# Kernel optimization log

Measured on AMD Instinct MI355X. Metric: run time of the kernel, lower is better.

Reference implementation:

```python
import jax, jax.numpy as jnp
import numpy as np

N_NODES = 100000
N_EDGES = 640000
D_IN = 128
D_HID = 128
D_OUT = 64


def gcn_conv(x, src, dst, ew, W, b, num_nodes):
    """GCNConv with add_self_loops=False: h = D^{-1/2} A D^{-1/2} (x W) + b.

    PyG gcn_norm: row, col = edge_index; deg = scatter_add(edge_weight, col);
    norm = deg^{-1/2}[row] * ew * deg^{-1/2}[col]; aggregate messages into col.
    """
    h = x @ W  # [N, d_out]
    deg = jax.ops.segment_sum(ew, dst, num_segments=num_nodes)  # [N]
    dinv = jnp.where(deg > 0, jax.lax.rsqrt(deg), 0.0)
    norm = dinv[src] * ew * dinv[dst]  # [E]
    out = jax.ops.segment_sum(norm[:, None] * h[src], dst, num_segments=num_nodes)
    return out + b


def setup_inputs() -> dict:
    key = jax.random.key(0)
    ks = jax.random.split(key, 9)
    x = jax.random.normal(ks[0], (N_NODES, D_IN), dtype=jnp.float32)
    edge_index = jax.random.randint(ks[1], (2, N_EDGES), 0, N_NODES, dtype=jnp.int64)
    edge_weight = jax.random.uniform(ks[2], (N_EDGES,), dtype=jnp.float32)
    def glorot(k, fan_in, fan_out):
        s = jnp.sqrt(6.0 / (fan_in + fan_out))
        return jax.random.uniform(k, (fan_in, fan_out), minval=-s, maxval=s, dtype=jnp.float32)
    W1 = glorot(ks[3], D_IN, D_HID); b1 = jnp.zeros((D_HID,), jnp.float32)
    W2 = glorot(ks[4], D_HID, D_HID); b2 = jnp.zeros((D_HID,), jnp.float32)
    W3 = glorot(ks[5], D_HID, D_OUT); b3 = jnp.zeros((D_OUT,), jnp.float32)
    return {"x": x, "edge_index": edge_index, "edge_weight": edge_weight,
            "W1": W1, "b1": b1, "W2": W2, "b2": b2, "W3": W3, "b3": b3}


def reference(x, edge_index, edge_weight, W1, b1, W2, b2, W3, b3):
    src, dst = edge_index[0], edge_index[1]
    n = x.shape[0]
    embeddings = []
    h = gcn_conv(x, src, dst, edge_weight, W1, b1, n)
    h = jax.nn.relu(h)
    embeddings.append(h)
    h = gcn_conv(h, src, dst, edge_weight, W2, b2, n)
    h = jax.nn.relu(h)
    embeddings.append(h)
    h = gcn_conv(h, src, dst, edge_weight, W3, b3, n)
    embeddings.append(h)
    return tuple(embeddings)
```

## Files before the change

kernel.cpp:

```cpp
#include <hip/hip_runtime.h>

#define NN 100000
#define NE 640000

typedef unsigned int uint32;
typedef __attribute__((ext_vector_type(8))) short short8;
typedef __attribute__((ext_vector_type(4))) float f32x4;

static __device__ __forceinline__ ushort f2bf(float f) {
    uint32 u = __float_as_uint(f);
    u = (u + 0x7fffu + ((u >> 16) & 1u)) >> 16;
    return (ushort)u;
}
static __device__ __forceinline__ float bf2f(uint32 bits16) {
    return __uint_as_float(bits16 << 16);
}
static __device__ __forceinline__ uint32 pack2(float a, float b) {
    return (uint32)f2bf(a) | ((uint32)f2bf(b) << 16);
}


__global__ void k_deg_hist(const int* __restrict__ dst, const float* __restrict__ ew,
                           float* __restrict__ deg, int* __restrict__ cnt, int E) {
    int e = blockIdx.x * blockDim.x + threadIdx.x;
    if (e < E) {
        int d = dst[e];
        atomicAdd(&deg[d], ew[e]);
        atomicAdd(&cnt[d], 1);
    }
}


__global__ void k_scan1(const int* __restrict__ cnt, int* __restrict__ rp,
                        int* __restrict__ bsum, int n) {
    __shared__ int tsum[256];
    const int base = blockIdx.x * 1024;
    const int t = threadIdx.x;
    int v[4], s = 0;
#pragma unroll
    for (int j = 0; j < 4; ++j) {
        int idx = base + t * 4 + j;
        v[j] = (idx < n) ? cnt[idx] : 0;
        s += v[j];
    }
    tsum[t] = s;
    __syncthreads();
    for (int off = 1; off < 256; off <<= 1) {
        int x = (t >= off) ? tsum[t - off] : 0;
        __syncthreads();
        tsum[t] += x;
        __syncthreads();
    }
    int excl = (t > 0) ? tsum[t - 1] : 0;
#pragma unroll
    for (int j = 0; j < 4; ++j) {
        int idx = base + t * 4 + j;
        if (idx < n) rp[idx] = excl;
        excl += v[j];
    }
    if (t == 255) bsum[blockIdx.x] = tsum[255];
}

__global__ void k_scan2(int* __restrict__ bsum, int nb) {
    __shared__ int sh[256];
    int t = threadIdx.x;
    sh[t] = (t < nb) ? bsum[t] : 0;
    __syncthreads();
    for (int off = 1; off < 256; off <<= 1) {
        int x = (t >= off) ? sh[t - off] : 0;
        __syncthreads();
        sh[t] += x;
        __syncthreads();
    }
    if (t < nb) bsum[t] = (t > 0) ? sh[t - 1] : 0;
}

__global__ void k_scan3(int* __restrict__ rp, const int* __restrict__ bsum,
                        int* __restrict__ cursor, float* __restrict__ deg, int n) {
    int i = blockIdx.x * blockDim.x + threadIdx.x;
    if (i < n) {
        int v = rp[i] + bsum[i >> 10];
        rp[i] = v;
        cursor[i] = v;
        float d = deg[i];
        deg[i] = (d > 0.f) ? rsqrtf(d) : 0.f;
    }
    if (i == 0) rp[n] = NE;
}

__global__ void k_fill(const int* __restrict__ src, const int* __restrict__ dst,
                       const float* __restrict__ ew, const float* __restrict__ dinv,
                       int* __restrict__ cursor, uint2* __restrict__ ep, int E) {
    int e = blockIdx.x * blockDim.x + threadIdx.x;
    if (e < E) {
        int s = src[e], d = dst[e];
        int pos = atomicAdd(&cursor[d], 1);
        float nv = dinv[s] * ew[e] * dinv[d];
        ep[pos] = make_uint2((uint32)s, __float_as_uint(nv));
    }
}

__global__ void k_prepW_all(const float* __restrict__ W1, const float* __restrict__ W2,
                            const float* __restrict__ W3, ushort* __restrict__ wt1,
                            ushort* __restrict__ wt2, ushort* __restrict__ wt3) {
    int o = blockIdx.x * blockDim.x + threadIdx.x;
    if (o < 16384) {
        int col = o >> 7, k = o & 127;
        wt1[o] = f2bf(W1[k * 128 + col]);
    } else if (o < 32768) {
        int oo = o - 16384;
        int col = oo >> 7, k = oo & 127;
        wt2[oo] = f2bf(W2[k * 128 + col]);
    } else if (o < 40960) {
        int oo = o - 32768;
        int col = oo >> 7, k = oo & 127;
        wt3[oo] = f2bf(W3[k * 64 + col]);
    }
}

template <int NOUT>
__global__ __launch_bounds__(256) void k_gemm_mfma(const float* __restrict__ X,
                                                   const ushort* __restrict__ Wt,
                                                   ushort* __restrict__ H, int N) {
    __shared__ char smem[64 * 256 + NOUT * 256];
    char* xs = smem;
    char* wt = smem + 64 * 256;
    const int tid = threadIdx.x;
    const int row0 = blockIdx.x * 64;

    const uint4* Wt4 = reinterpret_cast<const uint4*>(Wt);
#pragma unroll
    for (int i = 0; i < NOUT / 16; ++i) {
        int id = tid + 256 * i;
        int col = id >> 4, c4 = id & 15;
        uint4 v = Wt4[id];
        *reinterpret_cast<uint4*>(wt + col * 256 + ((c4 * 16) ^ ((col & 7) << 4))) = v;
    }
#pragma unroll
    for (int i = 0; i < 8; ++i) {
        int id = tid + 256 * i;
        int r = id >> 5, c4 = id & 31;
        int gr = row0 + r;
        float4 v = make_float4(0.f, 0.f, 0.f, 0.f);
        if (gr < N) v = *reinterpret_cast<const float4*>(&X[(size_t)gr * 128 + c4 * 4]);
        uint2 pk;
        pk.x = pack2(v.x, v.y);
        pk.y = pack2(v.z, v.w);
        *reinterpret_cast<uint2*>(xs + r * 256 + ((c4 * 8) ^ ((r & 7) << 4))) = pk;
    }
    __syncthreads();

    const int w = tid >> 6, lane = tid & 63;
    const int rl = w * 16 + (lane & 15);
    const int kg = lane >> 4;
    f32x4 acc[NOUT / 16];
#pragma unroll
    for (int ct = 0; ct < NOUT / 16; ++ct) acc[ct] = (f32x4){0.f, 0.f, 0.f, 0.f};

#pragma unroll
    for (int ks = 0; ks < 4; ++ks) {
        const int kb = ks * 64 + kg * 16;
        short8 a = *reinterpret_cast<const short8*>(xs + rl * 256 + (kb ^ ((rl & 7) << 4)));
#pragma unroll
        for (int ct = 0; ct < NOUT / 16; ++ct) {
            int col = ct * 16 + (lane & 15);
            short8 bfr = *reinterpret_cast<const short8*>(wt + col * 256 + (kb ^ ((col & 7) << 4)));
            acc[ct] = __builtin_amdgcn_mfma_f32_16x16x32_bf16(a, bfr, acc[ct], 0, 0, 0);
        }
    }
#pragma unroll
    for (int ct = 0; ct < NOUT / 16; ++ct) {
        int col = ct * 16 + (lane & 15);
#pragma unroll
        for (int r = 0; r < 4; ++r) {
            int gr = row0 + w * 16 + (lane >> 4) * 4 + r;
            if (gr < N) H[(size_t)gr * NOUT + col] = f2bf(acc[ct][r]);
        }
    }
}

template <int WAVES, int RELU>
__global__ void k_agg128(const int* __restrict__ rp, const uint2* __restrict__ ep,
                         const ushort* __restrict__ H, const float* __restrict__ b,
                         float* __restrict__ out, int N) {
    const int wave = threadIdx.x >> 6;
    const int lane = threadIdx.x & 63;
    const int n = blockIdx.x * WAVES + wave;
    if (n >= N) return;
    const int e0 = rp[n], e1 = rp[n + 1];
    const int slot = lane >> 4;
    const int l16 = lane & 15;

    const float4 b0 = *reinterpret_cast<const float4*>(&b[l16 * 8]);
    const float4 b1 = *reinterpret_cast<const float4*>(&b[l16 * 8 + 4]);

    float a[8] = {};
    int e = e0 + slot;
    if (e < e1) {
        uint2 p = ep[e];
        for (;;) {
            const int en = e + 4;
            uint2 pn = ep[en];
            float w = __uint_as_float(p.y);
            uint4 hv = *reinterpret_cast<const uint4*>(&H[(size_t)p.x * 128 + l16 * 8]);
            a[0] = fmaf(w, bf2f(hv.x & 0xffffu), a[0]);
            a[1] = fmaf(w, bf2f(hv.x >> 16), a[1]);
            a[2] = fmaf(w, bf2f(hv.y & 0xffffu), a[2]);
            a[3] = fmaf(w, bf2f(hv.y >> 16), a[3]);
            a[4] = fmaf(w, bf2f(hv.z & 0xffffu), a[4]);
            a[5] = fmaf(w, bf2f(hv.z >> 16), a[5]);
            a[6] = fmaf(w, bf2f(hv.w & 0xffffu), a[6]);
            a[7] = fmaf(w, bf2f(hv.w >> 16), a[7]);
            e = en;
            if (e >= e1) break;
            p = pn;
        }
    }
#pragma unroll
    for (int j = 0; j < 8; ++j) {
        a[j] += __shfl_xor(a[j], 32);
        a[j] += __shfl_xor(a[j], 16);
    }
    if (lane < 16) {
        float4 o0 = make_float4(a[0] + b0.x, a[1] + b0.y, a[2] + b0.z, a[3] + b0.w);
        float4 o1 = make_float4(a[4] + b1.x, a[5] + b1.y, a[6] + b1.z, a[7] + b1.w);
        if (RELU) {
            o0.x = fmaxf(o0.x, 0.f); o0.y = fmaxf(o0.y, 0.f);
            o0.z = fmaxf(o0.z, 0.f); o0.w = fmaxf(o0.w, 0.f);
            o1.x = fmaxf(o1.x, 0.f); o1.y = fmaxf(o1.y, 0.f);
            o1.z = fmaxf(o1.z, 0.f); o1.w = fmaxf(o1.w, 0.f);
        }
        float* op = &out[(size_t)n * 128 + l16 * 8];
        *reinterpret_cast<float4*>(op) = o0;
        *reinterpret_cast<float4*>(op + 4) = o1;
    }
}

template <int WAVES, int RELU>
__global__ void k_agg64(const int* __restrict__ rp, const uint2* __restrict__ ep,
                        const ushort* __restrict__ H, const float* __restrict__ b,
                        float* __restrict__ out, int N) {
    const int wave = threadIdx.x >> 6;
    const int lane = threadIdx.x & 63;
    const int n = blockIdx.x * WAVES + wave;
    if (n >= N) return;
    const int e0 = rp[n], e1 = rp[n + 1];
    const int slot = lane >> 3;
    const int l8 = lane & 7;

    const float4 b0 = *reinterpret_cast<const float4*>(&b[l8 * 8]);
    const float4 b1 = *reinterpret_cast<const float4*>(&b[l8 * 8 + 4]);

    float a[8] = {};
    int e = e0 + slot;
    if (e < e1) {
        uint2 p = ep[e];
        for (;;) {
            const int en = e + 8;
            uint2 pn = ep[en];
            float w = __uint_as_float(p.y);
            uint4 hv = *reinterpret_cast<const uint4*>(&H[(size_t)p.x * 64 + l8 * 8]);
            a[0] = fmaf(w, bf2f(hv.x & 0xffffu), a[0]);
            a[1] = fmaf(w, bf2f(hv.x >> 16), a[1]);
            a[2] = fmaf(w, bf2f(hv.y & 0xffffu), a[2]);
            a[3] = fmaf(w, bf2f(hv.y >> 16), a[3]);
            a[4] = fmaf(w, bf2f(hv.z & 0xffffu), a[4]);
            a[5] = fmaf(w, bf2f(hv.z >> 16), a[5]);
            a[6] = fmaf(w, bf2f(hv.w & 0xffffu), a[6]);
            a[7] = fmaf(w, bf2f(hv.w >> 16), a[7]);
            e = en;
            if (e >= e1) break;
            p = pn;
        }
    }
#pragma unroll
    for (int j = 0; j < 8; ++j) {
        a[j] += __shfl_xor(a[j], 8);
        a[j] += __shfl_xor(a[j], 16);
        a[j] += __shfl_xor(a[j], 32);
    }
    if (lane < 8) {
        float4 o0 = make_float4(a[0] + b0.x, a[1] + b0.y, a[2] + b0.z, a[3] + b0.w);
        float4 o1 = make_float4(a[4] + b1.x, a[5] + b1.y, a[6] + b1.z, a[7] + b1.w);
        if (RELU) {
            o0.x = fmaxf(o0.x, 0.f); o0.y = fmaxf(o0.y, 0.f);
            o0.z = fmaxf(o0.z, 0.f); o0.w = fmaxf(o0.w, 0.f);
            o1.x = fmaxf(o1.x, 0.f); o1.y = fmaxf(o1.y, 0.f);
            o1.z = fmaxf(o1.z, 0.f); o1.w = fmaxf(o1.w, 0.f);
        }
        float* op = &out[(size_t)n * 64 + l8 * 8];
        *reinterpret_cast<float4*>(op) = o0;
        *reinterpret_cast<float4*>(op + 4) = o1;
    }
}


extern "C" void kernel_launch(void* const* d_in, const int* in_sizes, int n_in,
                              void* d_out, int out_size, void* d_ws, size_t ws_size,
                              hipStream_t stream) {
    const float* x  = (const float*)d_in[0];
    const int*   ei = (const int*)d_in[1];
    const float* ew = (const float*)d_in[2];
    const float* W1 = (const float*)d_in[3];
    const float* b1 = (const float*)d_in[4];
    const float* W2 = (const float*)d_in[5];
    const float* b2 = (const float*)d_in[6];
    const float* W3 = (const float*)d_in[7];
    const float* b3 = (const float*)d_in[8];

    const int* src = ei;
    const int* dst = ei + NE;

    float*  ws    = (float*)d_ws;
    float*  deg   = ws;
    int*    cnt   = (int*)(ws + NN);
    int*    rp    = (int*)(ws + 2 * NN);
    int*    bsum  = (int*)(ws + 3 * NN + 64);
    uint2*  ep    = (uint2*)(ws + 3 * NN + 256);
    ushort* h1    = (ushort*)(ws + 3 * NN + 256 + 2 * NE);
    ushort* h2    = h1 + (size_t)NN * 128;
    ushort* h3    = h1;
    ushort* wt1   = h2 + (size_t)NN * 128;
    ushort* wt2   = wt1 + 128 * 128;
    ushort* wt3   = wt2 + 128 * 128;

    float* out0 = (float*)d_out;
    float* out1 = out0 + NN * 128;
    float* out2 = out1 + NN * 128;

    const int B = 256;
    const int NB_SCAN = (NN + 1023) / 1024;

    k_prepW_all<<<(40960 + B - 1) / B, B, 0, stream>>>(W1, W2, W3, wt1, wt2, wt3);

    hipMemsetAsync(deg, 0, 2 * NN * sizeof(float), stream);
    k_deg_hist<<<(NE + B - 1) / B, B, 0, stream>>>(dst, ew, deg, cnt, NE);
    k_scan1<<<NB_SCAN, 256, 0, stream>>>(cnt, rp, bsum, NN);
    k_scan2<<<1, 256, 0, stream>>>(bsum, NB_SCAN);
    k_scan3<<<(NN + B - 1) / B, B, 0, stream>>>(rp, bsum, cnt, deg, NN);
    k_fill<<<(NE + B - 1) / B, B, 0, stream>>>(src, dst, ew, deg, cnt, ep, NE);

    const int GB = (NN + 63) / 64;

    k_gemm_mfma<128><<<GB, 256, 0, stream>>>(x, wt1, h1, NN);
    k_agg128<4, 1><<<(NN + 3) / 4, 256, 0, stream>>>(rp, ep, h1, b1, out0, NN);

    k_gemm_mfma<128><<<GB, 256, 0, stream>>>(out0, wt2, h2, NN);
    k_agg128<4, 1><<<(NN + 3) / 4, 256, 0, stream>>>(rp, ep, h2, b2, out1, NN);

    k_gemm_mfma<64><<<GB, 256, 0, stream>>>(out1, wt3, h3, NN);
    k_agg64<4, 0><<<(NN + 3) / 4, 256, 0, stream>>>(rp, ep, h3, b3, out2, NN);
}
```

Before: 278.6 us.

## Fuse weight prep with zeroing and co-launch degree histogram with first GEMM

Folds the degree/count memset into the weight-conversion kernel, and merges the degree histogram into the first GEMM launch as extra blocks, so the independent histogram atomics overlap with the layer-1 GEMM. The histogram now processes four edges per thread with vector loads. This cuts two launches and the serial dependency of histogram then GEMM. The catch is larger shared memory for the histogram blocks, which may lower occupancy, and contention between atomics and GEMM traffic.

```diff
diff --git a/kernel.cpp b/kernel.cpp
--- a/kernel.cpp
+++ b/kernel.cpp
@@ -2,6 +2,10 @@
 
 #define NN 100000
 #define NE 640000
+#define GB1 ((NN + 63) / 64)
+#define HB1 (NE / 4 / 256)
+#define PWB 160
+#define ZB  ((2 * NN + 255) / 256)
 
 typedef unsigned int uint32;
 typedef __attribute__((ext_vector_type(8))) short short8;
@@ -19,15 +23,120 @@
     return (uint32)f2bf(a) | ((uint32)f2bf(b) << 16);
 }
 
-
-__global__ void k_deg_hist(const int* __restrict__ dst, const float* __restrict__ ew,
-                           float* __restrict__ deg, int* __restrict__ cnt, int E) {
-    int e = blockIdx.x * blockDim.x + threadIdx.x;
-    if (e < E) {
-        int d = dst[e];
-        atomicAdd(&deg[d], ew[e]);
-        atomicAdd(&cnt[d], 1);
-    }
+__global__ void k_prep_zero(const float* __restrict__ W1, const float* __restrict__ W2,
+                            const float* __restrict__ W3, ushort* __restrict__ wt1,
+                            ushort* __restrict__ wt2, ushort* __restrict__ wt3,
+                            int* __restrict__ degcnt) {
+    const int b = blockIdx.x;
+    if (b < PWB) {
+        int o = b * 256 + threadIdx.x;
+        if (o < 16384) {
+            int col = o >> 7, k = o & 127;
+            wt1[o] = f2bf(W1[k * 128 + col]);
+        } else if (o < 32768) {
+            int oo = o - 16384;
+            int col = oo >> 7, k = oo & 127;
+            wt2[oo] = f2bf(W2[k * 128 + col]);
+        } else if (o < 40960) {
+            int oo = o - 32768;
+            int col = oo >> 7, k = oo & 127;
+            wt3[oo] = f2bf(W3[k * 64 + col]);
+        }
+    } else {
+        int i = (b - PWB) * 256 + threadIdx.x;
+        if (i < 2 * NN) degcnt[i] = 0;
+    }
+}
+
+template <int NOUT>
+static __device__ __forceinline__ void gemm_body(const float* __restrict__ X,
+                                                 const ushort* __restrict__ Wt,
+                                                 ushort* __restrict__ H, int N,
+                                                 int bid, int tid, char* smem) {
+    char* xs = smem;
+    char* wt = smem + 64 * 256;
+    const int row0 = bid * 64;
+
+    const uint4* Wt4 = reinterpret_cast<const uint4*>(Wt);
+#pragma unroll
+    for (int i = 0; i < NOUT / 16; ++i) {
+        int id = tid + 256 * i;
+        int col = id >> 4, c4 = id & 15;
+        uint4 v = Wt4[id];
+        *reinterpret_cast<uint4*>(wt + col * 256 + ((c4 * 16) ^ ((col & 7) << 4))) = v;
+    }
+#pragma unroll
+    for (int i = 0; i < 8; ++i) {
+        int id = tid + 256 * i;
+        int r = id >> 5, c4 = id & 31;
+        int gr = row0 + r;
+        float4 v = make_float4(0.f, 0.f, 0.f, 0.f);
+        if (gr < N) v = *reinterpret_cast<const float4*>(&X[(size_t)gr * 128 + c4 * 4]);
+        uint2 pk;
+        pk.x = pack2(v.x, v.y);
+        pk.y = pack2(v.z, v.w);
+        *reinterpret_cast<uint2*>(xs + r * 256 + ((c4 * 8) ^ ((r & 7) << 4))) = pk;
+    }
+    __syncthreads();
+
+    const int w = tid >> 6, lane = tid & 63;
+    const int rl = w * 16 + (lane & 15);
+    const int kg = lane >> 4;
+    f32x4 acc[NOUT / 16];
+#pragma unroll
+    for (int ct = 0; ct < NOUT / 16; ++ct) acc[ct] = (f32x4){0.f, 0.f, 0.f, 0.f};
+
+#pragma unroll
+    for (int ks = 0; ks < 4; ++ks) {
+        const int kb = ks * 64 + kg * 16;
+        short8 a = *reinterpret_cast<const short8*>(xs + rl * 256 + (kb ^ ((rl & 7) << 4)));
+#pragma unroll
+        for (int ct = 0; ct < NOUT / 16; ++ct) {
+            int col = ct * 16 + (lane & 15);
+            short8 bfr = *reinterpret_cast<const short8*>(wt + col * 256 + (kb ^ ((col & 7) << 4)));
+            acc[ct] = __builtin_amdgcn_mfma_f32_16x16x32_bf16(a, bfr, acc[ct], 0, 0, 0);
+        }
+    }
+#pragma unroll
+    for (int ct = 0; ct < NOUT / 16; ++ct) {
+        int col = ct * 16 + (lane & 15);
+#pragma unroll
+        for (int r = 0; r < 4; ++r) {
+            int gr = row0 + w * 16 + (lane >> 4) * 4 + r;
+            if (gr < N) H[(size_t)gr * NOUT + col] = f2bf(acc[ct][r]);
+        }
+    }
+}
+
+__global__ __launch_bounds__(256) void k_gemm1_hist(const float* __restrict__ X,
+                                                    const ushort* __restrict__ Wt1,
+                                                    ushort* __restrict__ H, int N,
+                                                    const int* __restrict__ dst,
+                                                    const float* __restrict__ ew,
+                                                    float* __restrict__ deg,
+                                                    int* __restrict__ cnt) {
+    __shared__ char smem[64 * 256 + 128 * 256];
+    if (blockIdx.x < GB1) {
+        gemm_body<128>(X, Wt1, H, N, blockIdx.x, threadIdx.x, smem);
+    } else {
+        int e0 = ((blockIdx.x - GB1) * 256 + threadIdx.x) * 4;
+        if (e0 < NE) {
+            int4 d4 = *reinterpret_cast<const int4*>(&dst[e0]);
+            float4 w4 = *reinterpret_cast<const float4*>(&ew[e0]);
+            atomicAdd(&deg[d4.x], w4.x); atomicAdd(&cnt[d4.x], 1);
+            atomicAdd(&deg[d4.y], w4.y); atomicAdd(&cnt[d4.y], 1);
+            atomicAdd(&deg[d4.z], w4.z); atomicAdd(&cnt[d4.z], 1);
+            atomicAdd(&deg[d4.w], w4.w); atomicAdd(&cnt[d4.w], 1);
+        }
+    }
+}
+
+template <int NOUT>
+__global__ __launch_bounds__(256) void k_gemm_mfma(const float* __restrict__ X,
+                                                   const ushort* __restrict__ Wt,
+                                                   ushort* __restrict__ H, int N) {
+    __shared__ char smem[64 * 256 + NOUT * 256];
+    gemm_body<NOUT>(X, Wt, H, N, blockIdx.x, threadIdx.x, smem);
 }
 
 
@@ -97,85 +206,6 @@
         int pos = atomicAdd(&cursor[d], 1);
         float nv = dinv[s] * ew[e] * dinv[d];
         ep[pos] = make_uint2((uint32)s, __float_as_uint(nv));
-    }
-}
-
-__global__ void k_prepW_all(const float* __restrict__ W1, const float* __restrict__ W2,
-                            const float* __restrict__ W3, ushort* __restrict__ wt1,
-                            ushort* __restrict__ wt2, ushort* __restrict__ wt3) {
-    int o = blockIdx.x * blockDim.x + threadIdx.x;
-    if (o < 16384) {
-        int col = o >> 7, k = o & 127;
-        wt1[o] = f2bf(W1[k * 128 + col]);
-    } else if (o < 32768) {
-        int oo = o - 16384;
-        int col = oo >> 7, k = oo & 127;
-        wt2[oo] = f2bf(W2[k * 128 + col]);
-    } else if (o < 40960) {
-        int oo = o - 32768;
-        int col = oo >> 7, k = oo & 127;
-        wt3[oo] = f2bf(W3[k * 64 + col]);
-    }
-}
-
-template <int NOUT>
-__global__ __launch_bounds__(256) void k_gemm_mfma(const float* __restrict__ X,
-                                                   const ushort* __restrict__ Wt,
-                                                   ushort* __restrict__ H, int N) {
-    __shared__ char smem[64 * 256 + NOUT * 256];
-    char* xs = smem;
-    char* wt = smem + 64 * 256;
-    const int tid = threadIdx.x;
-    const int row0 = blockIdx.x * 64;
-
-    const uint4* Wt4 = reinterpret_cast<const uint4*>(Wt);
-#pragma unroll
-    for (int i = 0; i < NOUT / 16; ++i) {
-        int id = tid + 256 * i;
-        int col = id >> 4, c4 = id & 15;
-        uint4 v = Wt4[id];
-        *reinterpret_cast<uint4*>(wt + col * 256 + ((c4 * 16) ^ ((col & 7) << 4))) = v;
-    }
-#pragma unroll
-    for (int i = 0; i < 8; ++i) {
-        int id = tid + 256 * i;
-        int r = id >> 5, c4 = id & 31;
-        int gr = row0 + r;
-        float4 v = make_float4(0.f, 0.f, 0.f, 0.f);
-        if (gr < N) v = *reinterpret_cast<const float4*>(&X[(size_t)gr * 128 + c4 * 4]);
-        uint2 pk;
-        pk.x = pack2(v.x, v.y);
-        pk.y = pack2(v.z, v.w);
-        *reinterpret_cast<uint2*>(xs + r * 256 + ((c4 * 8) ^ ((r & 7) << 4))) = pk;
-    }
-    __syncthreads();
-
-    const int w = tid >> 6, lane = tid & 63;
-    const int rl = w * 16 + (lane & 15);
-    const int kg = lane >> 4;
-    f32x4 acc[NOUT / 16];
-#pragma unroll
-    for (int ct = 0; ct < NOUT / 16; ++ct) acc[ct] = (f32x4){0.f, 0.f, 0.f, 0.f};
-
-#pragma unroll
-    for (int ks = 0; ks < 4; ++ks) {
-        const int kb = ks * 64 + kg * 16;
-        short8 a = *reinterpret_cast<const short8*>(xs + rl * 256 + (kb ^ ((rl & 7) << 4)));
-#pragma unroll
-        for (int ct = 0; ct < NOUT / 16; ++ct) {
-            int col = ct * 16 + (lane & 15);
-            short8 bfr = *reinterpret_cast<const short8*>(wt + col * 256 + (kb ^ ((col & 7) << 4)));
-            acc[ct] = __builtin_amdgcn_mfma_f32_16x16x32_bf16(a, bfr, acc[ct], 0, 0, 0);
-        }
-    }
-#pragma unroll
-    for (int ct = 0; ct < NOUT / 16; ++ct) {
-        int col = ct * 16 + (lane & 15);
-#pragma unroll
-        for (int r = 0; r < 4; ++r) {
-            int gr = row0 + w * 16 + (lane >> 4) * 4 + r;
-            if (gr < N) H[(size_t)gr * NOUT + col] = f2bf(acc[ct][r]);
-        }
     }
 }
 
@@ -331,23 +361,20 @@
     const int B = 256;
     const int NB_SCAN = (NN + 1023) / 1024;
 
-    k_prepW_all<<<(40960 + B - 1) / B, B, 0, stream>>>(W1, W2, W3, wt1, wt2, wt3);
-
-    hipMemsetAsync(deg, 0, 2 * NN * sizeof(float), stream);
-    k_deg_hist<<<(NE + B - 1) / B, B, 0, stream>>>(dst, ew, deg, cnt, NE);
+    k_prep_zero<<<PWB + ZB, B, 0, stream>>>(W1, W2, W3, wt1, wt2, wt3, (int*)deg);
+
+    k_gemm1_hist<<<GB1 + HB1, 256, 0, stream>>>(x, wt1, h1, NN, dst, ew, deg, cnt);
+
     k_scan1<<<NB_SCAN, 256, 0, stream>>>(cnt, rp, bsum, NN);
     k_scan2<<<1, 256, 0, stream>>>(bsum, NB_SCAN);
     k_scan3<<<(NN + B - 1) / B, B, 0, stream>>>(rp, bsum, cnt, deg, NN);
     k_fill<<<(NE + B - 1) / B, B, 0, stream>>>(src, dst, ew, deg, cnt, ep, NE);
 
-    const int GB = (NN + 63) / 64;
-
-    k_gemm_mfma<128><<<GB, 256, 0, stream>>>(x, wt1, h1, NN);
     k_agg128<4, 1><<<(NN + 3) / 4, 256, 0, stream>>>(rp, ep, h1, b1, out0, NN);
 
-    k_gemm_mfma<128><<<GB, 256, 0, stream>>>(out0, wt2, h2, NN);
+    k_gemm_mfma<128><<<GB1, 256, 0, stream>>>(out0, wt2, h2, NN);
     k_agg128<4, 1><<<(NN + 3) / 4, 256, 0, stream>>>(rp, ep, h2, b2, out1, NN);
 
-    k_gemm_mfma<64><<<GB, 256, 0, stream>>>(out1, wt3, h3, NN);
+    k_gemm_mfma<64><<<GB1, 256, 0, stream>>>(out1, wt3, h3, NN);
     k_agg64<4, 0><<<(NN + 3) / 4, 256, 0, stream>>>(rp, ep, h3, b3, out2, NN);
 }
```

Result: faster. 272.6 us (-2.1%).
